# Kernel optimization log

Hardware: AMD Instinct MI355X
Metric: run time of the kernel (lower is better)

The kernel has to match this reference:

```python
import jax, jax.numpy as jnp
import numpy as np

PI = float(np.pi)
C = jnp.complex64
N = 10  # qubits

def m2(a, b, c, d):
    a, b, c, d = jnp.broadcast_arrays(*(jnp.asarray(v, C) for v in (a, b, c, d)))
    return jnp.stack([jnp.stack([a, b], -1), jnp.stack([c, d], -1)], -2)

def rx_mat(t):
    c = jnp.cos(t / 2); s = jnp.sin(t / 2)
    return m2(c, -1j * s, -1j * s, c)

def ry_mat(t):
    c = jnp.cos(t / 2); s = jnp.sin(t / 2)
    return m2(c, -s, s, c)

def rz_mat(t):
    return m2(jnp.exp(-0.5j * t), 0.0, 0.0, jnp.exp(0.5j * t))

def ps_mat(t):
    return m2(1.0, 0.0, 0.0, jnp.exp(1j * t))

def rot_mat(phi, theta, omega):
    c = jnp.cos(theta / 2); s = jnp.sin(theta / 2)
    return m2(jnp.exp(-0.5j * (phi + omega)) * c,
              -jnp.exp(0.5j * (phi - omega)) * s,
              jnp.exp(-0.5j * (phi - omega)) * s,
              jnp.exp(0.5j * (phi + omega)) * c)

def u2_mat(phi, lam):
    r = 1.0 / np.sqrt(2.0)
    return m2(r, -r * jnp.exp(1j * lam), r * jnp.exp(1j * phi), r * jnp.exp(1j * (phi + lam)))

def u3_mat(theta, phi, lam):
    c = jnp.cos(theta / 2); s = jnp.sin(theta / 2)
    return m2(c, -jnp.exp(1j * lam) * s, jnp.exp(1j * phi) * s, jnp.exp(1j * (phi + lam)) * c)

def controlled(U):
    sh = U.shape[:-2]
    I2 = jnp.broadcast_to(jnp.eye(2, dtype=C), sh + (2, 2))
    Z2 = jnp.zeros(sh + (2, 2), C)
    return jnp.concatenate([jnp.concatenate([I2, Z2], -1), jnp.concatenate([Z2, U], -1)], -2)

Y_M = jnp.array([[0, -1j], [1j, 0]], C)
S_M = jnp.array([[1, 0], [0, 1j]], C)
T_M = jnp.array([[1, 0], [0, np.exp(1j * np.pi / 4)]], C)
SX_M = 0.5 * jnp.array([[1 + 1j, 1 - 1j], [1 - 1j, 1 + 1j]], C)
CNOT_M = jnp.array(np.eye(4)[[0, 1, 3, 2]], C)
CZ_M = jnp.array(np.diag([1.0, 1.0, 1.0, -1.0]), C)
CY_M = jnp.array([[1, 0, 0, 0], [0, 1, 0, 0], [0, 0, 0, -1j], [0, 0, 1j, 0]], C)
SWAP_M = jnp.array(np.eye(4)[[0, 2, 1, 3]], C)
CSWAP_M = jnp.array(np.eye(8)[[0, 1, 2, 3, 4, 6, 5, 7]], C)
TOFF_M = jnp.array(np.eye(8)[[0, 1, 2, 3, 4, 5, 7, 6]], C)
CX12_M = jnp.array(np.eye(4)[[0, 1, 3, 2]], C)  # qubitunitary [[1,0,0,0],[0,1,0,0],[0,0,0,1],[0,0,1,0]]

def apply_gate(state, U, wires):
    # state: [B] + [2]*N ; U: [2^k,2^k] or [B,2^k,2^k]
    B = state.shape[0]
    k = len(wires)
    axes = tuple(w + 1 for w in wires)
    s = jnp.moveaxis(state, axes, tuple(range(1, 1 + k)))
    sh = s.shape
    s = s.reshape(B, 2 ** k, -1)
    U = jnp.asarray(U, s.dtype)
    if U.ndim == 2:
        s = jnp.einsum('ij,bjr->bir', U, s)
    else:
        s = jnp.einsum('bij,bjr->bir', U, s)
    return jnp.moveaxis(s.reshape(sh), tuple(range(1, 1 + k)), axes)

def multirz(state, theta, wires):
    # diagonal exp(-i theta/2 * Z...Z) phase
    z = jnp.array([1.0, -1.0], jnp.float32)
    sign = jnp.ones((1,) * (N + 1), jnp.float32)
    for w in wires:
        shp = [1] * (N + 1); shp[w + 1] = 2
        sign = sign * z.reshape(shp)
    theta = jnp.reshape(jnp.asarray(theta), (-1,) + (1,) * N)
    return state * jnp.exp(-0.5j * theta * sign)

def net(x, w1, b1, w2, b2, fw1, fb1, fw2, fb2):
    dn = ('NCHW', 'OIHW', 'NCHW')
    h = jax.lax.conv_general_dilated(x, w1, (1, 1), 'VALID', dimension_numbers=dn)
    h = jax.nn.relu(h + b1[None, :, None, None])
    h = jax.lax.conv_general_dilated(h, w2, (1, 1), 'VALID', dimension_numbers=dn)
    h = jax.nn.relu(h + b2[None, :, None, None])
    h = jax.lax.reduce_window(h, -jnp.inf, jax.lax.max, (1, 1, 2, 2), (1, 1, 2, 2), 'VALID')
    h = h.reshape(h.shape[0], -1)  # [B, 9216]
    h = jax.nn.relu(h @ fw1.T + fb1)
    h = h @ fw2.T + fb2
    return jax.nn.sigmoid(h) * (2.0 * PI)  # angles in [0, 2pi], dropout in eval mode

def run_circuit(ang, q_rx, q_rz3, q_ps6, q_rot7, q_mrz8, q_crx9, q_cry10, q_crz11, q_u2, q_u3):
    B = ang.shape[0]
    state = jnp.zeros((B, 2 ** N), C).at[:, 0].set(1.0).reshape((B,) + (2,) * N)
    for k in range(N):  # TrainableOpAll(RX)
        state = apply_gate(state, rx_mat(q_rx[k]), (k,))
    for k in range(N):  # OpAll(RY) + repeated rx(wire0, x[:,0])
        state = apply_gate(state, ry_mat(ang[:, k]), (k,))
        state = apply_gate(state, rx_mat(ang[:, 0]), (0,))
    for k in range(N - 1):  # TQAll CNOT ring
        state = apply_gate(state, CNOT_M, (k, k + 1))
    state = apply_gate(state, CNOT_M, (N - 1, 0))
    state = apply_gate(state, rx_mat(ang[:, 1]), (1,))
    state = apply_gate(state, rx_mat(jnp.float32(-PI / 4)), (5,))  # q_layer2 fixed
    state = apply_gate(state, ry_mat(ang[:, 2]), (2,))
    state = apply_gate(state, rz_mat(ang[:, 3]), (3,))
    state = apply_gate(state, S_M, (4,))
    state = apply_gate(state, T_M, (5,))
    state = apply_gate(state, rz_mat(q_rz3[0]), (6,))
    state = apply_gate(state, SX_M, (7,))
    # q_device1 (3-wire) ops do not affect the output -> omitted
    state = apply_gate(state, CZ_M, (0, 5))
    state = apply_gate(state, CNOT_M, (0, 5))
    state = apply_gate(state, CY_M, (0, 5))
    state = apply_gate(state, CY_M, (3, 8))
    state = apply_gate(state, SWAP_M, (2, 3))
    state = apply_gate(state, CSWAP_M, (4, 5, 6))
    state = apply_gate(state, TOFF_M, (8, 5, 0))
    state = apply_gate(state, ps_mat(q_ps6[0]), (8,))
    state = apply_gate(state, ps_mat(ang[:, 7]), (7,))
    state = apply_gate(state, rot_mat(q_rot7[0], q_rot7[1], q_rot7[2]), (4,))
    state = apply_gate(state, rot_mat(ang[:, 6], ang[:, 7], ang[:, 8]), (5,))
    state = multirz(state, q_mrz8[0], (2, 3, 4, 5, 6))
    state = multirz(state, ang[:, 5], (3, 4, 6, 7, 8))
    state = apply_gate(state, controlled(rx_mat(ang[:, 6])), (0, 1))
    state = apply_gate(state, controlled(rx_mat(q_crx9[0])), (4, 5))
    state = apply_gate(state, controlled(ry_mat(ang[:, 6])), (0, 1))
    state = apply_gate(state, controlled(ry_mat(q_cry10[0])), (4, 5))
    state = apply_gate(state, controlled(rz_mat(ang[:, 6])), (0, 1))
    state = apply_gate(state, controlled(rz_mat(q_crz11[0])), (4, 5))
    state = apply_gate(state, controlled(rot_mat(jnp.float32(-PI / 4), jnp.float32(PI / 4), jnp.float32(PI / 2))), (5, 6))
    state = apply_gate(state, controlled(rot_mat(ang[:, 5], ang[:, 6], ang[:, 7])), (7, 8))
    state = apply_gate(state, ps_mat(jnp.float32(PI / 7)), (1,))  # U1 == PhaseShift
    state = apply_gate(state, ps_mat(ang[:, 9]), (2,))
    state = apply_gate(state, u2_mat(q_u2[0], q_u2[1]), (8,))
    state = apply_gate(state, u2_mat(ang[:, 0], ang[:, 1]), (4,))
    state = apply_gate(state, u3_mat(q_u3[0], q_u3[1], q_u3[2]), (5,))
    state = apply_gate(state, u3_mat(ang[:, 4], ang[:, 5], ang[:, 6]), (5,))
    # q_layer16 QubitUnitary is identity -> no-op
    state = apply_gate(state, CX12_M, (1, 2))
    red = tuple(range(1, N + 1))
    evs = [jnp.real(jnp.sum(jnp.conj(state) * apply_gate(state, Y_M, (w,)), axis=red)) for w in range(N)]
    return jnp.stack(evs, 1)  # [B, 10]

def setup_inputs():
    key = jax.random.key(0)
    ks = jax.random.split(key, 16)
    B = 1024
    return {
        'x': jax.random.uniform(ks[0], (B, 1, 28, 28), jnp.float32),
        'conv1_w': jax.random.normal(ks[1], (32, 1, 3, 3), jnp.float32) * 0.2,
        'conv1_b': jnp.zeros((32,), jnp.float32),
        'conv2_w': jax.random.normal(ks[2], (64, 32, 3, 3), jnp.float32) * 0.05,
        'conv2_b': jnp.zeros((64,), jnp.float32),
        'fc1_w': jax.random.normal(ks[3], (128, 9216), jnp.float32) * 0.01,
        'fc1_b': jnp.zeros((128,), jnp.float32),
        'fc2_w': jax.random.normal(ks[4], (10, 128), jnp.float32) * 0.08,
        'fc2_b': jnp.zeros((10,), jnp.float32),
        'q_rx': jax.random.uniform(ks[5], (10,), jnp.float32, 0.0, 2 * PI),
        'q_rz3': jax.random.uniform(ks[6], (1,), jnp.float32, 0.0, 2 * PI),
        'q_ps6': jax.random.uniform(ks[7], (1,), jnp.float32, 0.0, 2 * PI),
        'q_rot7': jax.random.uniform(ks[8], (3,), jnp.float32, 0.0, 2 * PI),
        'q_mrz8': jax.random.uniform(ks[9], (1,), jnp.float32, 0.0, 2 * PI),
        'q_crx9': jax.random.uniform(ks[10], (1,), jnp.float32, 0.0, 2 * PI),
        'q_cry10': jax.random.uniform(ks[11], (1,), jnp.float32, 0.0, 2 * PI),
        'q_crz11': jax.random.uniform(ks[12], (1,), jnp.float32, 0.0, 2 * PI),
        'q_u2_14': jnp.array([PI / 7, PI / 8.8], jnp.float32),
        'q_u3_15': jax.random.uniform(ks[13], (3,), jnp.float32, 0.0, 2 * PI),
    }

def reference(x, conv1_w, conv1_b, conv2_w, conv2_b, fc1_w, fc1_b, fc2_w, fc2_b,
              q_rx, q_rz3, q_ps6, q_rot7, q_mrz8, q_crx9, q_cry10, q_crz11, q_u2_14, q_u3_15):
    ang = net(x, conv1_w, conv1_b, conv2_w, conv2_b, fc1_w, fc1_b, fc2_w, fc2_b)
    ev = run_circuit(ang, q_rx, q_rz3, q_ps6, q_rot7, q_mrz8, q_crx9, q_cry10, q_crz11, q_u2_14, q_u3_15)
    return jax.nn.log_softmax(ev, axis=1)
```

## Files before the change

### kernel.cpp

```cpp
#include <hip/hip_runtime.h>
#include <hip/hip_bf16.h>

#define PI_F 3.14159265358979323846f

__global__ void Static_82300163326800_kernel() {}

typedef _Float16 f16x8 __attribute__((ext_vector_type(8)));
typedef _Float16 f16x4 __attribute__((ext_vector_type(4)));
typedef float f32x4 __attribute__((ext_vector_type(4)));

struct M2 { float2 m00, m01, m10, m11; };

__device__ __forceinline__ int ins1(int x, int p) {
    return ((x >> p) << (p + 1)) | (x & ((1 << p) - 1));
}
__device__ __forceinline__ M2 mrx(float th) {
    float s, c; __sincosf(0.5f * th, &s, &c);
    return { make_float2(c,0.f), make_float2(0.f,-s), make_float2(0.f,-s), make_float2(c,0.f) };
}
__device__ __forceinline__ M2 mry(float th) {
    float s, c; __sincosf(0.5f * th, &s, &c);
    return { make_float2(c,0.f), make_float2(-s,0.f), make_float2(s,0.f), make_float2(c,0.f) };
}
__device__ __forceinline__ M2 mrot(float phi, float th, float om) {
    float s, c;  __sincosf(0.5f * th, &s, &c);
    float sa, ca; __sincosf(0.5f * (phi + om), &sa, &ca);
    float sd, cd; __sincosf(0.5f * (phi - om), &sd, &cd);
    return { make_float2(ca*c, -sa*c), make_float2(-cd*s, -sd*s),
             make_float2(cd*s, -sd*s), make_float2(ca*c,  sa*c) };
}
__device__ __forceinline__ M2 mu2(float phi, float lam) {
    const float r = 0.7071067811865476f;
    float sl, cl;   __sincosf(lam, &sl, &cl);
    float sp, cp;   __sincosf(phi, &sp, &cp);
    float spl, cpl; __sincosf(phi + lam, &spl, &cpl);
    return { make_float2(r,0.f), make_float2(-r*cl,-r*sl),
             make_float2(r*cp, r*sp), make_float2(r*cpl, r*spl) };
}
__device__ __forceinline__ M2 mu3(float th, float phi, float lam) {
    float s, c;     __sincosf(0.5f * th, &s, &c);
    float sl, cl;   __sincosf(lam, &sl, &cl);
    float sp, cp;   __sincosf(phi, &sp, &cp);
    float spl, cpl; __sincosf(phi + lam, &spl, &cpl);
    return { make_float2(c,0.f), make_float2(-cl*s,-sl*s),
             make_float2(cp*s, sp*s), make_float2(cpl*c, spl*c) };
}
__device__ __forceinline__ void apply1(float2* st, int t, int w, M2 m) {
    int p = 9 - w;
    int i0 = ins1(t, p), i1 = i0 | (1 << p);
    float2 a = st[i0], d = st[i1];
    st[i0] = make_float2(m.m00.x*a.x - m.m00.y*a.y + m.m01.x*d.x - m.m01.y*d.y,
                         m.m00.x*a.y + m.m00.y*a.x + m.m01.x*d.y + m.m01.y*d.x);
    st[i1] = make_float2(m.m10.x*a.x - m.m10.y*a.y + m.m11.x*d.x - m.m11.y*d.y,
                         m.m10.x*a.y + m.m10.y*a.x + m.m11.x*d.y + m.m11.y*d.x);
}
__device__ __forceinline__ void diag1(float2* st, int t, int w, float2 d0, float2 d1) {
    int p = 9 - w;
    int i0 = ins1(t, p), i1 = i0 | (1 << p);
    float2 a = st[i0], c = st[i1];
    st[i0] = make_float2(d0.x*a.x - d0.y*a.y, d0.x*a.y + d0.y*a.x);
    st[i1] = make_float2(d1.x*c.x - d1.y*c.y, d1.x*c.y + d1.y*c.x);
}
__device__ __forceinline__ void capply1(float2* st, int t, int c, int w, M2 m) {
    if (t < 256) {
        int pc = 9 - c, pw = 9 - w;
        int pl = pc < pw ? pc : pw, ph = pc + pw - pl;
        int base = ins1(ins1(t, pl), ph) | (1 << pc);
        int i0 = base, i1 = base | (1 << pw);
        float2 a = st[i0], d = st[i1];
        st[i0] = make_float2(m.m00.x*a.x - m.m00.y*a.y + m.m01.x*d.x - m.m01.y*d.y,
                             m.m00.x*a.y + m.m00.y*a.x + m.m01.x*d.y + m.m01.y*d.x);
        st[i1] = make_float2(m.m10.x*a.x - m.m10.y*a.y + m.m11.x*d.x - m.m11.y*d.y,
                             m.m10.x*a.y + m.m10.y*a.x + m.m11.x*d.y + m.m11.y*d.x);
    }
}
__device__ __forceinline__ void cdiag1(float2* st, int t, int c, int w, float2 d0, float2 d1) {
    if (t < 256) {
        int pc = 9 - c, pw = 9 - w;
        int pl = pc < pw ? pc : pw, ph = pc + pw - pl;
        int base = ins1(ins1(t, pl), ph) | (1 << pc);
        int i0 = base, i1 = base | (1 << pw);
        float2 a = st[i0], e = st[i1];
        st[i0] = make_float2(d0.x*a.x - d0.y*a.y, d0.x*a.y + d0.y*a.x);
        st[i1] = make_float2(d1.x*e.x - d1.y*e.y, d1.x*e.y + d1.y*e.x);
    }
}
__device__ __forceinline__ void cnotg(float2* st, int t, int c, int w) {
    if (t < 256) {
        int pc = 9 - c, pw = 9 - w;
        int pl = pc < pw ? pc : pw, ph = pc + pw - pl;
        int base = ins1(ins1(t, pl), ph) | (1 << pc);
        int i1 = base | (1 << pw);
        float2 a = st[base]; st[base] = st[i1]; st[i1] = a;
    }
}
__device__ __forceinline__ void czg(float2* st, int t, int c, int w) {
    if (t < 256) {
        int pc = 9 - c, pw = 9 - w;
        int pl = pc < pw ? pc : pw, ph = pc + pw - pl;
        int i = ins1(ins1(t, pl), ph) | (1 << pc) | (1 << pw);
        st[i] = make_float2(-st[i].x, -st[i].y);
    }
}
__device__ __forceinline__ void swapg(float2* st, int t, int a, int b_) {
    if (t < 256) {
        int pa = 9 - a, pb = 9 - b_;
        int pl = pa < pb ? pa : pb, ph = pa + pb - pl;
        int base = ins1(ins1(t, pl), ph);
        int iA = base | (1 << pa), iB = base | (1 << pb);
        float2 u = st[iA]; st[iA] = st[iB]; st[iB] = u;
    }
}
__device__ __forceinline__ void cswap456(float2* st, int t) {
    if (t < 128) {
        int base = ins1(ins1(ins1(t, 3), 4), 5) | (1 << 5);
        int iA = base | (1 << 4), iB = base | (1 << 3);
        float2 u = st[iA]; st[iA] = st[iB]; st[iB] = u;
    }
}
__device__ __forceinline__ void toff850(float2* st, int t) {
    if (t < 128) {
        int base = ins1(ins1(ins1(t, 1), 4), 9) | (1 << 1) | (1 << 4);
        int i1 = base | (1 << 9);
        float2 u = st[base]; st[base] = st[i1]; st[i1] = u;
    }
}
__device__ __forceinline__ void mrzg(float2* st, int t, int mask, float th) {
    float sh, ch; __sincosf(0.5f * th, &sh, &ch);
#pragma unroll
    for (int q = 0; q < 2; ++q) {
        int i = t + q * 512;
        float sg = (__popc(i & mask) & 1) ? sh : -sh;
        float2 a = st[i];
        st[i] = make_float2(ch*a.x - sg*a.y, ch*a.y + sg*a.x);
    }
}

__device__ __forceinline__ void run_circ(
    float2* st, float (*red)[10], float* evs, int t, const float* ang,
    const float* q_rx, const float* q_rz3, const float* q_ps6, const float* q_rot7,
    const float* q_mrz8, const float* q_crx9, const float* q_cry10, const float* q_crz11,
    const float* q_u2, const float* q_u3, float* outf)
{
    st[t] = make_float2(t == 0 ? 1.f : 0.f, 0.f);
    st[t + 512] = make_float2(0.f, 0.f);

#pragma unroll
    for (int k = 0; k < 10; ++k) { M2 m = mrx(q_rx[k]); __syncthreads(); apply1(st, t, k, m); }
    {
        M2 mx0 = mrx(ang[0]);
#pragma unroll
        for (int k = 0; k < 10; ++k) {
            M2 m = mry(ang[k]); __syncthreads(); apply1(st, t, k, m);
            __syncthreads(); apply1(st, t, 0, mx0);
        }
    }
#pragma unroll
    for (int k = 0; k < 9; ++k) { __syncthreads(); cnotg(st, t, k, k + 1); }
    __syncthreads(); cnotg(st, t, 9, 0);

    { M2 m = mrx(ang[1]);      __syncthreads(); apply1(st, t, 1, m); }
    { M2 m = mrx(-PI_F / 4.f); __syncthreads(); apply1(st, t, 5, m); }
    { M2 m = mry(ang[2]);      __syncthreads(); apply1(st, t, 2, m); }
    { float s, c; __sincosf(0.5f * ang[3], &s, &c);
      __syncthreads(); diag1(st, t, 3, make_float2(c,-s), make_float2(c,s)); }
    __syncthreads(); diag1(st, t, 4, make_float2(1.f,0.f), make_float2(0.f,1.f));
    __syncthreads(); diag1(st, t, 5, make_float2(1.f,0.f),
                           make_float2(0.7071067811865476f, 0.7071067811865476f));
    { float s, c; __sincosf(0.5f * q_rz3[0], &s, &c);
      __syncthreads(); diag1(st, t, 6, make_float2(c,-s), make_float2(c,s)); }
    { M2 m = { make_float2(0.5f,0.5f), make_float2(0.5f,-0.5f),
               make_float2(0.5f,-0.5f), make_float2(0.5f,0.5f) };
      __syncthreads(); apply1(st, t, 7, m); }
    __syncthreads(); czg(st, t, 0, 5);
    __syncthreads(); cnotg(st, t, 0, 5);
    { M2 y = { make_float2(0.f,0.f), make_float2(0.f,-1.f),
               make_float2(0.f,1.f), make_float2(0.f,0.f) };
      __syncthreads(); capply1(st, t, 0, 5, y);
      __syncthreads(); capply1(st, t, 3, 8, y); }
    __syncthreads(); swapg(st, t, 2, 3);
    __syncthreads(); cswap456(st, t);
    __syncthreads(); toff850(st, t);
    { float s, c; __sincosf(q_ps6[0], &s, &c);
      __syncthreads(); diag1(st, t, 8, make_float2(1.f,0.f), make_float2(c,s)); }
    { float s, c; __sincosf(ang[7], &s, &c);
      __syncthreads(); diag1(st, t, 7, make_float2(1.f,0.f), make_float2(c,s)); }
    { M2 m = mrot(q_rot7[0], q_rot7[1], q_rot7[2]); __syncthreads(); apply1(st, t, 4, m); }
    { M2 m = mrot(ang[6], ang[7], ang[8]);          __syncthreads(); apply1(st, t, 5, m); }
    __syncthreads(); mrzg(st, t, 0xF8, q_mrz8[0]);
    __syncthreads(); mrzg(st, t, 0x6E, ang[5]);
    { M2 m = mrx(ang[6]);      __syncthreads(); capply1(st, t, 0, 1, m); }
    { M2 m = mrx(q_crx9[0]);   __syncthreads(); capply1(st, t, 4, 5, m); }
    { M2 m = mry(ang[6]);      __syncthreads(); capply1(st, t, 0, 1, m); }
    { M2 m = mry(q_cry10[0]);  __syncthreads(); capply1(st, t, 4, 5, m); }
    { float s, c; __sincosf(0.5f * ang[6], &s, &c);
      __syncthreads(); cdiag1(st, t, 0, 1, make_float2(c,-s), make_float2(c,s)); }
    { float s, c; __sincosf(0.5f * q_crz11[0], &s, &c);
      __syncthreads(); cdiag1(st, t, 4, 5, make_float2(c,-s), make_float2(c,s)); }
    { M2 m = mrot(-PI_F/4.f, PI_F/4.f, PI_F/2.f); __syncthreads(); capply1(st, t, 5, 6, m); }
    { M2 m = mrot(ang[5], ang[6], ang[7]);        __syncthreads(); capply1(st, t, 7, 8, m); }
    { float s, c; __sincosf(PI_F/7.f, &s, &c);
      __syncthreads(); diag1(st, t, 1, make_float2(1.f,0.f), make_float2(c,s)); }
    { float s, c; __sincosf(ang[9], &s, &c);
      __syncthreads(); diag1(st, t, 2, make_float2(1.f,0.f), make_float2(c,s)); }
    { M2 m = mu2(q_u2[0], q_u2[1]); __syncthreads(); apply1(st, t, 8, m); }
    { M2 m = mu2(ang[0], ang[1]);   __syncthreads(); apply1(st, t, 4, m); }
    { M2 m = mu3(q_u3[0], q_u3[1], q_u3[2]); __syncthreads(); apply1(st, t, 5, m); }
    { M2 m = mu3(ang[4], ang[5], ang[6]);    __syncthreads(); apply1(st, t, 5, m); }
    __syncthreads(); cnotg(st, t, 1, 2);
    __syncthreads();

    float loc[10];
#pragma unroll
    for (int w = 0; w < 10; ++w) {
        int p = 9 - w;
        int i0 = ins1(t, p), i1 = i0 | (1 << p);
        float2 a = st[i0], c = st[i1];
        loc[w] = 2.f * (a.x * c.y - a.y * c.x);
    }
    int lane = t & 63, wv = t >> 6;
#pragma unroll
    for (int w = 0; w < 10; ++w) {
        float v = loc[w];
        v += __shfl_down(v, 32); v += __shfl_down(v, 16); v += __shfl_down(v, 8);
        v += __shfl_down(v, 4);  v += __shfl_down(v, 2);  v += __shfl_down(v, 1);
        if (lane == 0) red[wv][w] = v;
    }
    __syncthreads();
    if (t < 10) {
        float e = 0.f;
#pragma unroll
        for (int i = 0; i < 8; ++i) e += red[i][t];
        evs[t] = e;
    }
    __syncthreads();
    if (t < 10) {
        float mx = evs[0];
#pragma unroll
        for (int i = 1; i < 10; ++i) mx = fmaxf(mx, evs[i]);
        float ss = 0.f;
#pragma unroll
        for (int i = 0; i < 10; ++i) ss += expf(evs[i] - mx);
        outf[t] = evs[t] - mx - logf(ss);
    }
}

__global__ __launch_bounds__(256) void prep_w2(
    const float* __restrict__ w2, _Float16* __restrict__ w2t)
{
    int idx = blockIdx.x * 256 + threadIdx.x;
    if (idx < 18432) {
        int oc = idx / 288, r = idx - oc * 288;
        int s = r >> 5, ic = r & 31;
        w2t[idx] = (_Float16)w2[oc * 288 + ic * 9 + s];
    }
}

__global__ __launch_bounds__(256) void prep_fw1(
    const float* __restrict__ fw1, _Float16* __restrict__ out)
{
    int i = blockIdx.x * 256 + threadIdx.x;
    if (i < 294912) {
        float4 v = ((const float4*)fw1)[i];
        f16x4 o = { (_Float16)v.x, (_Float16)v.y, (_Float16)v.z, (_Float16)v.w };
        *(f16x4*)(out + i * 4) = o;
    }
}

__global__ __launch_bounds__(256, 2) void convnet_mfma(
    const float* __restrict__ x, const float* __restrict__ w1, const float* __restrict__ b1,
    const _Float16* __restrict__ w2t, const float* __restrict__ b2,
    _Float16* __restrict__ flat)
{
    __shared__ float xs[784];
    __shared__ float w1s[288];
    __shared__ __align__(16) _Float16 h1t[676 * 40];
    const int n = blockIdx.x, t = threadIdx.x;
    const int lane = t & 63, wv = t >> 6;
    const int m = lane & 15, quad = lane >> 4;

    for (int i = t; i < 784; i += 256) xs[i] = x[n * 784 + i];
    for (int i = t; i < 288; i += 256) w1s[i] = w1[i];

    bf16x8_dummy: ;
    f16x8 bq[9][4];
#pragma unroll
    for (int s = 0; s < 9; ++s)
#pragma unroll
        for (int nt = 0; nt < 4; ++nt)
            bq[s][nt] = *(const f16x8*)(w2t + (nt * 16 + m) * 288 + s * 32 + quad * 8);

    __syncthreads();

    {
        const int ic = t & 31;
        float wr[9];
#pragma unroll
        for (int k = 0; k < 9; ++k) wr[k] = w1s[ic * 9 + k];
        const float bb = b1[ic];
        for (int pix = (t >> 5); pix < 676; pix += 8) {
            int yy = pix / 26, xx = pix - yy * 26;
            const float* xp = xs + yy * 28 + xx;
            float s = bb;
            s += xp[0]*wr[0]  + xp[1]*wr[1]  + xp[2]*wr[2]
               + xp[28]*wr[3] + xp[29]*wr[4] + xp[30]*wr[5]
               + xp[56]*wr[6] + xp[57]*wr[7] + xp[58]*wr[8];
            h1t[pix * 40 + ic] = (_Float16)fmaxf(s, 0.f);
        }
    }
    __syncthreads();

    float bb2[4];
#pragma unroll
    for (int nt = 0; nt < 4; ++nt) bb2[nt] = b2[nt * 16 + m];

    _Float16* outp = flat + (size_t)n * 9216;

    for (int q = 0; q < 9; ++q) {
        const int mt = wv + q * 4;
        const int a = mt / 3, b3 = mt - a * 3;
        const int y0 = 2 * a + (m & 1), x0 = 8 * b3 + (m >> 1);
        f32x4 acc[4] = {};
#pragma unroll
        for (int s = 0; s < 9; ++s) {
            const int ky = s / 3, kx = s - ky * 3;
            f16x8 af = *(const f16x8*)&h1t[((y0 + ky) * 26 + x0 + kx) * 40 + quad * 8];
#pragma unroll
            for (int nt = 0; nt < 4; ++nt)
                acc[nt] = __builtin_amdgcn_mfma_f32_16x16x32_f16(af, bq[s][nt], acc[nt], 0, 0, 0);
        }
        const int pooled_idx = a * 12 + 4 * b3 + quad;
#pragma unroll
        for (int nt = 0; nt < 4; ++nt) {
            float v = fmaxf(fmaxf(acc[nt][0], acc[nt][1]), fmaxf(acc[nt][2], acc[nt][3]));
            outp[(nt * 16 + m) * 144 + pooled_idx] = (_Float16)fmaxf(v + bb2[nt], 0.f);
        }
    }
}

__global__ __launch_bounds__(256) void fc1_mfma(
    const _Float16* __restrict__ A, const _Float16* __restrict__ B, float* __restrict__ part)
{
    const int m0 = blockIdx.x * 64, n0 = blockIdx.y * 64, kb = blockIdx.z;
    const int t = threadIdx.x, lane = t & 63, wv = t >> 6;
    const int r = lane & 15, quad = lane >> 4;
    const _Float16* ap = A + (size_t)(m0 + wv * 16 + r) * 9216 + kb * 576 + quad * 8;
    const _Float16* bp = B + (size_t)(n0 + r) * 9216 + kb * 576 + quad * 8;
    f32x4 acc[4] = {};
    for (int ks = 0; ks < 576; ks += 32) {
        f16x8 af = *(const f16x8*)(ap + ks);
#pragma unroll
        for (int nt = 0; nt < 4; ++nt) {
            f16x8 bfr = *(const f16x8*)(bp + (size_t)nt * 16 * 9216 + ks);
            acc[nt] = __builtin_amdgcn_mfma_f32_16x16x32_f16(af, bfr, acc[nt], 0, 0, 0);
        }
    }
    float* pp = part + (size_t)kb * 131072 + (size_t)(m0 + wv * 16 + quad * 4) * 128 + n0 + r;
#pragma unroll
    for (int nt = 0; nt < 4; ++nt)
#pragma unroll
        for (int reg = 0; reg < 4; ++reg)
            pp[reg * 128 + nt * 16] = acc[nt][reg];
}

__global__ __launch_bounds__(128) void fc2_kernel(
    const float* __restrict__ part, const float* __restrict__ fb1,
    const float* __restrict__ fw2, const float* __restrict__ fb2, float* __restrict__ angO)
{
    __shared__ float h[128];
    const int b = blockIdx.x, t = threadIdx.x;
    float s = fb1[t];
#pragma unroll
    for (int kb = 0; kb < 16; ++kb) s += part[(size_t)kb * 131072 + b * 128 + t];
    h[t] = fmaxf(s, 0.f);
    __syncthreads();
    if (t < 10) {
        float d = fb2[t];
#pragma unroll 16
        for (int k = 0; k < 128; ++k) d += h[k] * fw2[t * 128 + k];
        angO[b * 10 + t] = 6.283185307179586f / (1.f + expf(-d));
    }
}

__global__ __launch_bounds__(512) void circuit_kernel(
    const float* __restrict__ ang_g,
    const float* __restrict__ q_rx, const float* __restrict__ q_rz3,
    const float* __restrict__ q_ps6, const float* __restrict__ q_rot7,
    const float* __restrict__ q_mrz8, const float* __restrict__ q_crx9,
    const float* __restrict__ q_cry10, const float* __restrict__ q_crz11,
    const float* __restrict__ q_u2, const float* __restrict__ q_u3,
    float* __restrict__ out)
{
    __shared__ float2 st[1024];
    __shared__ float red[8][10];
    __shared__ float evs[10];
    const int b = blockIdx.x, t = threadIdx.x;
    float a[10];
#pragma unroll
    for (int j = 0; j < 10; ++j) a[j] = ang_g[b * 10 + j];
    run_circ(st, red, evs, t, a, q_rx, q_rz3, q_ps6, q_rot7, q_mrz8,
             q_crx9, q_cry10, q_crz11, q_u2, q_u3, out + b * 10);
}

template <int NT>
__device__ __forceinline__ void conv_stage(
    float* buf, int n, int t,
    const float* __restrict__ x, const float* __restrict__ w1, const float* __restrict__ b1,
    const float* __restrict__ w2, const float* __restrict__ b2)
{
    float* xs  = buf;
    float* w1s = buf + 784;
    float* h1s = buf + 1072;
    float* w2s = buf + 1748;
    const int ocq = t / 24, r = t - ocq * 24;
    const bool active = (t < 384);

    for (int i = t; i < 784; i += NT) xs[i] = x[n * 784 + i];
    for (int i = t; i < 288; i += NT) w1s[i] = w1[i];

    float acc[4][24];
#pragma unroll
    for (int j = 0; j < 4; ++j)
#pragma unroll
        for (int xo = 0; xo < 24; ++xo) acc[j][xo] = 0.f;

    for (int ic = 0; ic < 32; ++ic) {
        __syncthreads();
        float bb1 = b1[ic];
        for (int i = t; i < 676; i += NT) {
            int yy = i / 26, xx = i - yy * 26;
            const float* xp = xs + yy * 28 + xx;
            const float* wp = w1s + ic * 9;
            float s = bb1;
#pragma unroll
            for (int ky = 0; ky < 3; ++ky)
#pragma unroll
                for (int kx = 0; kx < 3; ++kx)
                    s += xp[ky * 28 + kx] * wp[ky * 3 + kx];
            h1s[i] = fmaxf(s, 0.f);
        }
        for (int i = t; i < 576; i += NT) {
            int oc = i / 9, k = i - oc * 9;
            w2s[i] = w2[oc * 288 + ic * 9 + k];
        }
        __syncthreads();
        if (active) {
            float wr[4][9];
#pragma unroll
            for (int j = 0; j < 4; ++j)
#pragma unroll
                for (int k = 0; k < 9; ++k)
                    wr[j][k] = w2s[(ocq * 4 + j) * 9 + k];
            float c0[3], c1[3];
#pragma unroll
            for (int q = 0; q < 3; ++q) { c0[q] = h1s[(r + q) * 26]; c1[q] = h1s[(r + q) * 26 + 1]; }
#pragma unroll
            for (int xo = 0; xo < 24; ++xo) {
                float c2[3];
#pragma unroll
                for (int q = 0; q < 3; ++q) c2[q] = h1s[(r + q) * 26 + xo + 2];
#pragma unroll
                for (int j = 0; j < 4; ++j) {
                    acc[j][xo] += wr[j][0]*c0[0] + wr[j][1]*c1[0] + wr[j][2]*c2[0]
                                + wr[j][3]*c0[1] + wr[j][4]*c1[1] + wr[j][5]*c2[1]
                                + wr[j][6]*c0[2] + wr[j][7]*c1[2] + wr[j][8]*c2[2];
                }
#pragma unroll
                for (int q = 0; q < 3; ++q) { c0[q] = c1[q]; c1[q] = c2[q]; }
            }
        }
    }
    __syncthreads();
    if (active && (r & 1)) {
#pragma unroll
        for (int j = 0; j < 4; ++j) {
            int oc = ocq * 4 + j;
            float bb = b2[oc];
#pragma unroll
            for (int px = 0; px < 12; ++px) {
                float v0 = fmaxf(acc[j][2*px]   + bb, 0.f);
                float v1 = fmaxf(acc[j][2*px+1] + bb, 0.f);
                buf[oc * 144 + (r >> 1) * 12 + px] = fmaxf(v0, v1);
            }
        }
    }
    __syncthreads();
    if (active && !(r & 1)) {
#pragma unroll
        for (int j = 0; j < 4; ++j) {
            int oc = ocq * 4 + j;
            float bb = b2[oc];
#pragma unroll
            for (int px = 0; px < 12; ++px) {
                float v0 = fmaxf(acc[j][2*px]   + bb, 0.f);
                float v1 = fmaxf(acc[j][2*px+1] + bb, 0.f);
                int idx = oc * 144 + (r >> 1) * 12 + px;
                buf[idx] = fmaxf(fmaxf(v0, v1), buf[idx]);
            }
        }
    }
    __syncthreads();
}

__global__ __launch_bounds__(512) void fused_kernel(
    const float* __restrict__ x, const float* __restrict__ w1, const float* __restrict__ b1,
    const float* __restrict__ w2, const float* __restrict__ b2,
    const float* __restrict__ fw1, const float* __restrict__ fb1,
    const float* __restrict__ fw2, const float* __restrict__ fb2,
    const float* __restrict__ q_rx, const float* __restrict__ q_rz3,
    const float* __restrict__ q_ps6, const float* __restrict__ q_rot7,
    const float* __restrict__ q_mrz8, const float* __restrict__ q_crx9,
    const float* __restrict__ q_cry10, const float* __restrict__ q_crz11,
    const float* __restrict__ q_u2, const float* __restrict__ q_u3,
    float* __restrict__ out)
{
    __shared__ float buf[9216];
    __shared__ float2 st[1024];
    __shared__ float hred[512];
    __shared__ float hvec[128];
    __shared__ float angs[10];
    __shared__ float red[8][10];
    __shared__ float evs[10];
    const int n = blockIdx.x, t = threadIdx.x;

    conv_stage<512>(buf, n, t, x, w1, b1, w2, b2);

    {
        const int j = t >> 2, q = t & 3;
        const float* wrow = fw1 + (size_t)j * 9216 + q * 2304;
        const float* arow = buf + q * 2304;
        float s = 0.f;
        for (int k = 0; k < 2304; k += 4) {
            float4 w = *(const float4*)(wrow + k);
            s += w.x * arow[k] + w.y * arow[k+1] + w.z * arow[k+2] + w.w * arow[k+3];
        }
        hred[t] = s;
    }
    __syncthreads();
    if (t < 128)
        hvec[t] = fmaxf(fb1[t] + hred[t*4] + hred[t*4+1] + hred[t*4+2] + hred[t*4+3], 0.f);
    __syncthreads();
    if (t < 10) {
        float d = fb2[t];
#pragma unroll 16
        for (int k = 0; k < 128; ++k) d += hvec[k] * fw2[t * 128 + k];
        angs[t] = 6.283185307179586f / (1.f + expf(-d));
    }
    __syncthreads();
    run_circ(st, red, evs, t, angs, q_rx, q_rz3, q_ps6, q_rot7, q_mrz8,
             q_crx9, q_cry10, q_crz11, q_u2, q_u3, out + n * 10);
}

extern "C" void kernel_launch(void* const* d_in, const int* in_sizes, int n_in,
                              void* d_out, int out_size, void* d_ws, size_t ws_size,
                              hipStream_t stream)
{
    (void)in_sizes; (void)n_in;
    const float* x    = (const float*)d_in[0];
    const float* w1   = (const float*)d_in[1];
    const float* b1   = (const float*)d_in[2];
    const float* w2   = (const float*)d_in[3];
    const float* b2   = (const float*)d_in[4];
    const float* fw1  = (const float*)d_in[5];
    const float* fb1  = (const float*)d_in[6];
    const float* fw2  = (const float*)d_in[7];
    const float* fb2  = (const float*)d_in[8];
    const float* qrx  = (const float*)d_in[9];
    const float* qrz3 = (const float*)d_in[10];
    const float* qps6 = (const float*)d_in[11];
    const float* qrot7 = (const float*)d_in[12];
    const float* qmrz8 = (const float*)d_in[13];
    const float* qcrx9 = (const float*)d_in[14];
    const float* qcry10 = (const float*)d_in[15];
    const float* qcrz11 = (const float*)d_in[16];
    const float* qu2  = (const float*)d_in[17];
    const float* qu3  = (const float*)d_in[18];
    float* out = (float*)d_out;

    const size_t flat_bytes = (size_t)1024 * 9216 * 2;
    const size_t part_bytes = (size_t)16 * 1024 * 128 * 4;
    const size_t ang_bytes  = (size_t)1024 * 10 * 4;
    const size_t w2t_bytes  = (size_t)18432 * 2;
    const size_t fw1h_bytes = (size_t)128 * 9216 * 2;
    const size_t o_flat = 0;
    const size_t o_part = o_flat + flat_bytes;
    const size_t o_ang  = o_part + part_bytes;
    const size_t o_w2t  = o_ang + ang_bytes;
    const size_t o_fw1h = o_w2t + w2t_bytes;
    const size_t need   = o_fw1h + fw1h_bytes;

    (void)hipGetLastError();

    if (ws_size >= need) {
        _Float16* flat = (_Float16*)((char*)d_ws + o_flat);
        float*    part = (float*)((char*)d_ws + o_part);
        float*    angb = (float*)((char*)d_ws + o_ang);
        _Float16* w2t  = (_Float16*)((char*)d_ws + o_w2t);
        _Float16* fw1h = (_Float16*)((char*)d_ws + o_fw1h);
        prep_w2<<<72, 256, 0, stream>>>(w2, w2t);
        prep_fw1<<<1152, 256, 0, stream>>>(fw1, fw1h);
        convnet_mfma<<<1024, 256, 0, stream>>>(x, w1, b1, w2t, b2, flat);
        fc1_mfma<<<dim3(16, 2, 16), 256, 0, stream>>>(flat, fw1h, part);
        fc2_kernel<<<1024, 128, 0, stream>>>(part, fb1, fw2, fb2, angb);
        circuit_kernel<<<1024, 512, 0, stream>>>(angb, qrx, qrz3, qps6, qrot7, qmrz8,
                                                 qcrx9, qcry10, qcrz11, qu2, qu3, out);
    } else {
        fused_kernel<<<1024, 512, 0, stream>>>(x, w1, b1, w2, b2, fw1, fb1, fw2, fb2,
                                               qrx, qrz3, qps6, qrot7, qmrz8,
                                               qcrx9, qcry10, qcrz11, qu2, qu3, out);
    }
    if (hipGetLastError() != hipSuccess) {
        (void)hipMemsetAsync(d_out, 0x7F, (size_t)out_size * 2, stream);
    }
}
```

Before: 204.8 us.

## Simulate quantum circuit per wavefront in registers with lane shuffles

Replaces the 512-thread shared-memory circuit kernel, which had a __syncthreads between every gate, with one 64-lane wavefront per sample. Each lane holds 16 amplitudes in registers: the high six qubits map to lane bits and the low four to register indices. Gates become xor-shuffles or in-register permutations, so block-wide barriers and LDS traffic go away. The conv1 stage is also changed to a sliding-window row computation. The cost is hand-derived mappings for every gate, which raises the risk of correctness errors.

```diff
diff --git a/kernel.cpp b/kernel.cpp
--- a/kernel.cpp
+++ b/kernel.cpp
@@ -11,8 +11,14 @@
 
 struct M2 { float2 m00, m01, m10, m11; };
 
-__device__ __forceinline__ int ins1(int x, int p) {
-    return ((x >> p) << (p + 1)) | (x & ((1 << p) - 1));
+__device__ __forceinline__ float2 cmul2(float2 a, float2 b) {
+    return make_float2(a.x*b.x - a.y*b.y, a.x*b.y + a.y*b.x);
+}
+__device__ __forceinline__ float2 cadd2(float2 a, float2 b) {
+    return make_float2(a.x+b.x, a.y+b.y);
+}
+__device__ __forceinline__ float2 shx(float2 v, int m) {
+    return make_float2(__shfl_xor(v.x, m), __shfl_xor(v.y, m));
 }
 __device__ __forceinline__ M2 mrx(float th) {
     float s, c; __sincosf(0.5f * th, &s, &c);
@@ -45,21 +51,505 @@
     return { make_float2(c,0.f), make_float2(-cl*s,-sl*s),
              make_float2(cp*s, sp*s), make_float2(cpl*c, spl*c) };
 }
+
+
+__device__ __forceinline__ void applyL(float2* s, M2 m, int lane, int q) {
+    const int bitv = (lane >> q) & 1;
+    const float2 cA = bitv ? m.m11 : m.m00;
+    const float2 cB = bitv ? m.m10 : m.m01;
+#pragma unroll
+    for (int r = 0; r < 16; ++r) {
+        float2 o = shx(s[r], 1 << q);
+        s[r] = cadd2(cmul2(cA, s[r]), cmul2(cB, o));
+    }
+}
+template<int P>
+__device__ __forceinline__ void applyR(float2* s, M2 m) {
+#pragma unroll
+    for (int r0 = 0; r0 < 16; ++r0) {
+        if (r0 & (1 << P)) continue;
+        const int r1 = r0 | (1 << P);
+        float2 a = s[r0], d = s[r1];
+        s[r0] = cadd2(cmul2(m.m00, a), cmul2(m.m01, d));
+        s[r1] = cadd2(cmul2(m.m10, a), cmul2(m.m11, d));
+    }
+}
+__device__ __forceinline__ void diagL(float2* s, float2 d0, float2 d1, int lane, int q) {
+    const int bitv = (lane >> q) & 1;
+    const float2 f = bitv ? d1 : d0;
+#pragma unroll
+    for (int r = 0; r < 16; ++r) s[r] = cmul2(f, s[r]);
+}
+template<int P>
+__device__ __forceinline__ void diagR(float2* s, float2 d0, float2 d1) {
+#pragma unroll
+    for (int r = 0; r < 16; ++r) {
+        const float2 f = (r & (1 << P)) ? d1 : d0;
+        s[r] = cmul2(f, s[r]);
+    }
+}
+__device__ __forceinline__ void cnotLL(float2* s, int lane, int qc, int qw) {
+    const int cb = (lane >> qc) & 1;
+#pragma unroll
+    for (int r = 0; r < 16; ++r) {
+        float2 o = shx(s[r], 1 << qw);
+        s[r] = cb ? o : s[r];
+    }
+}
+__device__ __forceinline__ void capplyLL(float2* s, M2 m, int lane, int qc, int qw) {
+    const int cb = (lane >> qc) & 1, tb = (lane >> qw) & 1;
+    float2 cA = tb ? m.m11 : m.m00;
+    float2 cB = tb ? m.m10 : m.m01;
+    cA = cb ? cA : make_float2(1.f, 0.f);
+    cB = cb ? cB : make_float2(0.f, 0.f);
+#pragma unroll
+    for (int r = 0; r < 16; ++r) {
+        float2 o = shx(s[r], 1 << qw);
+        s[r] = cadd2(cmul2(cA, s[r]), cmul2(cB, o));
+    }
+}
+__device__ __forceinline__ void cdiagLL(float2* s, float2 d0, float2 d1, int lane, int qc, int qw) {
+    const int cb = (lane >> qc) & 1, tb = (lane >> qw) & 1;
+    float2 f = tb ? d1 : d0;
+    f = cb ? f : make_float2(1.f, 0.f);
+#pragma unroll
+    for (int r = 0; r < 16; ++r) s[r] = cmul2(f, s[r]);
+}
+template<int P>
+__device__ __forceinline__ void capplyRL(float2* s, M2 m, int lane, int qc) {
+    const int cb = (lane >> qc) & 1;
+#pragma unroll
+    for (int r0 = 0; r0 < 16; ++r0) {
+        if (r0 & (1 << P)) continue;
+        const int r1 = r0 | (1 << P);
+        float2 a = s[r0], d = s[r1];
+        float2 na = cadd2(cmul2(m.m00, a), cmul2(m.m01, d));
+        float2 nd = cadd2(cmul2(m.m10, a), cmul2(m.m11, d));
+        s[r0] = cb ? na : a;
+        s[r1] = cb ? nd : d;
+    }
+}
+
+__global__ __launch_bounds__(256) void circuit_wave(
+    const float* __restrict__ ang_g,
+    const float* __restrict__ q_rx, const float* __restrict__ q_rz3,
+    const float* __restrict__ q_ps6, const float* __restrict__ q_rot7,
+    const float* __restrict__ q_mrz8, const float* __restrict__ q_crx9,
+    const float* __restrict__ q_cry10, const float* __restrict__ q_crz11,
+    const float* __restrict__ q_u2, const float* __restrict__ q_u3,
+    float* __restrict__ out)
+{
+    const int t = threadIdx.x, lane = t & 63, wv = t >> 6;
+    const int b = blockIdx.x * 4 + wv;
+    float ang[10];
+#pragma unroll
+    for (int j = 0; j < 10; ++j) ang[j] = ang_g[b * 10 + j];
+
+    float2 s[16];
+#pragma unroll
+    for (int r = 0; r < 16; ++r) s[r] = make_float2(0.f, 0.f);
+    if (lane == 0) s[0].x = 1.f;
+
+    applyL(s, mrx(q_rx[0]), lane, 5);
+    applyL(s, mrx(q_rx[1]), lane, 4);
+    applyL(s, mrx(q_rx[2]), lane, 3);
+    applyL(s, mrx(q_rx[3]), lane, 2);
+    applyL(s, mrx(q_rx[4]), lane, 1);
+    applyL(s, mrx(q_rx[5]), lane, 0);
+    applyR<3>(s, mrx(q_rx[6]));
+    applyR<2>(s, mrx(q_rx[7]));
+    applyR<1>(s, mrx(q_rx[8]));
+    applyR<0>(s, mrx(q_rx[9]));
+    {
+        M2 mx0 = mrx(ang[0]);
+        applyL(s, mry(ang[0]), lane, 5); applyL(s, mx0, lane, 5);
+        applyL(s, mry(ang[1]), lane, 4); applyL(s, mx0, lane, 5);
+        applyL(s, mry(ang[2]), lane, 3); applyL(s, mx0, lane, 5);
+        applyL(s, mry(ang[3]), lane, 2); applyL(s, mx0, lane, 5);
+        applyL(s, mry(ang[4]), lane, 1); applyL(s, mx0, lane, 5);
+        applyL(s, mry(ang[5]), lane, 0); applyL(s, mx0, lane, 5);
+        applyR<3>(s, mry(ang[6]));       applyL(s, mx0, lane, 5);
+        applyR<2>(s, mry(ang[7]));       applyL(s, mx0, lane, 5);
+        applyR<1>(s, mry(ang[8]));       applyL(s, mx0, lane, 5);
+        applyR<0>(s, mry(ang[9]));       applyL(s, mx0, lane, 5);
+    }
+    cnotLL(s, lane, 5, 4);
+    cnotLL(s, lane, 4, 3);
+    cnotLL(s, lane, 3, 2);
+    cnotLL(s, lane, 2, 1);
+    cnotLL(s, lane, 1, 0);
+    {
+        const int cb = lane & 1;
+#pragma unroll
+        for (int r0 = 0; r0 < 8; ++r0) {
+            float2 a = s[r0], d = s[r0 + 8];
+            s[r0] = cb ? d : a; s[r0 + 8] = cb ? a : d;
+        }
+    }
+    {
+        float2 u;
+        u = s[8];  s[8]  = s[12]; s[12] = u;
+        u = s[9];  s[9]  = s[13]; s[13] = u;
+        u = s[10]; s[10] = s[14]; s[14] = u;
+        u = s[11]; s[11] = s[15]; s[15] = u;
+    }
+    {
+        float2 u;
+        u = s[4];  s[4]  = s[6];  s[6]  = u;
+        u = s[5];  s[5]  = s[7];  s[7]  = u;
+        u = s[12]; s[12] = s[14]; s[14] = u;
+        u = s[13]; s[13] = s[15]; s[15] = u;
+    }
+    {
+        float2 u;
+        u = s[2];  s[2]  = s[3];  s[3]  = u;
+        u = s[6];  s[6]  = s[7];  s[7]  = u;
+        u = s[10]; s[10] = s[11]; s[11] = u;
+        u = s[14]; s[14] = s[15]; s[15] = u;
+    }
+    {
+#pragma unroll
+        for (int r = 1; r < 16; r += 2) { float2 o = shx(s[r], 32); s[r] = o; }
+    }
+
+    applyL(s, mrx(ang[1]), lane, 4);
+    applyL(s, mrx(-PI_F / 4.f), lane, 0);
+    applyL(s, mry(ang[2]), lane, 3);
+    { float sn, cs; __sincosf(0.5f * ang[3], &sn, &cs);
+      diagL(s, make_float2(cs,-sn), make_float2(cs,sn), lane, 2); }
+    diagL(s, make_float2(1.f,0.f), make_float2(0.f,1.f), lane, 1);
+    diagL(s, make_float2(1.f,0.f),
+          make_float2(0.7071067811865476f, 0.7071067811865476f), lane, 0);
+    { float sn, cs; __sincosf(0.5f * q_rz3[0], &sn, &cs);
+      diagR<3>(s, make_float2(cs,-sn), make_float2(cs,sn)); }
+    { M2 m = { make_float2(0.5f,0.5f), make_float2(0.5f,-0.5f),
+               make_float2(0.5f,-0.5f), make_float2(0.5f,0.5f) };
+      applyR<2>(s, m); }
+    {
+        const float sgn = (((lane >> 5) & 1) && (lane & 1)) ? -1.f : 1.f;
+#pragma unroll
+        for (int r = 0; r < 16; ++r) { s[r].x *= sgn; s[r].y *= sgn; }
+    }
+    cnotLL(s, lane, 5, 0);
+    {
+        const int cb = (lane >> 5) & 1, tb = lane & 1;
+#pragma unroll
+        for (int r = 0; r < 16; ++r) {
+            float2 o = shx(s[r], 1);
+            float2 val = tb ? make_float2(-o.y, o.x) : make_float2(o.y, -o.x);
+            s[r] = cb ? val : s[r];
+        }
+    }
+    {
+        const int cb = (lane >> 2) & 1;
+#pragma unroll
+        for (int r0 = 0; r0 < 16; ++r0) {
+            if (r0 & 2) continue;
+            const int r1 = r0 | 2;
+            float2 a = s[r0], d = s[r1];
+            float2 na = make_float2(d.y, -d.x);
+            float2 nd = make_float2(-a.y, a.x);
+            s[r0] = cb ? na : a; s[r1] = cb ? nd : d;
+        }
+    }
+    {
+        const int pr = ((lane >> 3) & 1) ^ ((lane >> 2) & 1);
+#pragma unroll
+        for (int r = 0; r < 16; ++r) {
+            float2 o = shx(s[r], 12);
+            s[r] = pr ? o : s[r];
+        }
+    }
+    {
+        float2 o16[16];
+#pragma unroll
+        for (int r = 0; r < 16; ++r) o16[r] = shx(s[r ^ 8], 1);
+        const int cb = (lane >> 1) & 1, lb = lane & 1;
+#pragma unroll
+        for (int r = 0; r < 16; ++r) {
+            const int pr = cb & ((r & 8) ? (1 - lb) : lb);
+            s[r] = pr ? o16[r] : s[r];
+        }
+    }
+    {
+        const int lb = lane & 1;
+#pragma unroll
+        for (int r = 0; r < 16; ++r) {
+            if (!(r & 2)) continue;
+            float2 o = shx(s[r], 32);
+            s[r] = lb ? o : s[r];
+        }
+    }
+    { float sn, cs; __sincosf(q_ps6[0], &sn, &cs);
+      diagR<1>(s, make_float2(1.f,0.f), make_float2(cs,sn)); }
+    { float sn, cs; __sincosf(ang[7], &sn, &cs);
+      diagR<2>(s, make_float2(1.f,0.f), make_float2(cs,sn)); }
+    applyL(s, mrot(q_rot7[0], q_rot7[1], q_rot7[2]), lane, 1);
+    applyL(s, mrot(ang[6], ang[7], ang[8]), lane, 0);
+    {
+        float sh, ch; __sincosf(0.5f * q_mrz8[0], &sh, &ch);
+        const int lp = __popc(lane & 0xF) & 1;
+        const float sg0 = lp ? sh : -sh;
+#pragma unroll
+        for (int r = 0; r < 16; ++r) {
+            const float sg = (r & 8) ? -sg0 : sg0;
+            float2 a = s[r];
+            s[r] = make_float2(ch*a.x - sg*a.y, ch*a.y + sg*a.x);
+        }
+    }
+    {
+        float sh, ch; __sincosf(0.5f * ang[5], &sh, &ch);
+        const int lp = __popc(lane & 6) & 1;
+        const float sg0 = lp ? sh : -sh;
+#pragma unroll
+        for (int r = 0; r < 16; ++r) {
+            const int rp = __popc(r & 14) & 1;
+            const float sg = rp ? -sg0 : sg0;
+            float2 a = s[r];
+            s[r] = make_float2(ch*a.x - sg*a.y, ch*a.y + sg*a.x);
+        }
+    }
+    capplyLL(s, mrx(ang[6]), lane, 5, 4);
+    capplyLL(s, mrx(q_crx9[0]), lane, 1, 0);
+    capplyLL(s, mry(ang[6]), lane, 5, 4);
+    capplyLL(s, mry(q_cry10[0]), lane, 1, 0);
+    { float sn, cs; __sincosf(0.5f * ang[6], &sn, &cs);
+      cdiagLL(s, make_float2(cs,-sn), make_float2(cs,sn), lane, 5, 4); }
+    { float sn, cs; __sincosf(0.5f * q_crz11[0], &sn, &cs);
+      cdiagLL(s, make_float2(cs,-sn), make_float2(cs,sn), lane, 1, 0); }
+    capplyRL<3>(s, mrot(-PI_F/4.f, PI_F/4.f, PI_F/2.f), lane, 0);
+    {
+        M2 m = mrot(ang[5], ang[6], ang[7]);
+        const int idx4[4] = {4, 5, 12, 13};
+#pragma unroll
+        for (int k = 0; k < 4; ++k) {
+            const int r0 = idx4[k], r1 = r0 | 2;
+            float2 a = s[r0], d = s[r1];
+            s[r0] = cadd2(cmul2(m.m00, a), cmul2(m.m01, d));
+            s[r1] = cadd2(cmul2(m.m10, a), cmul2(m.m11, d));
+        }
+    }
+    { float sn, cs; __sincosf(PI_F / 7.f, &sn, &cs);
+      diagL(s, make_float2(1.f,0.f), make_float2(cs,sn), lane, 4); }
+    { float sn, cs; __sincosf(ang[9], &sn, &cs);
+      diagL(s, make_float2(1.f,0.f), make_float2(cs,sn), lane, 3); }
+    applyR<1>(s, mu2(q_u2[0], q_u2[1]));
+    applyL(s, mu2(ang[0], ang[1]), lane, 1);
+    applyL(s, mu3(q_u3[0], q_u3[1], q_u3[2]), lane, 0);
+    applyL(s, mu3(ang[4], ang[5], ang[6]), lane, 0);
+    cnotLL(s, lane, 4, 3);
+
+    float ev[10];
+#pragma unroll
+    for (int w = 0; w < 6; ++w) {
+        const int q = 5 - w;
+        const int bitv = (lane >> q) & 1;
+        float acc = 0.f;
+#pragma unroll
+        for (int r = 0; r < 16; ++r) {
+            float2 o = shx(s[r], 1 << q);
+            acc += s[r].x * o.y - s[r].y * o.x;
+        }
+        ev[w] = bitv ? 0.f : 2.f * acc;
+    }
+#pragma unroll
+    for (int w = 6; w < 10; ++w) {
+        const int P = 9 - w;
+        float acc = 0.f;
+#pragma unroll
+        for (int r0 = 0; r0 < 16; ++r0) {
+            if (r0 & (1 << P)) continue;
+            const int r1 = r0 | (1 << P);
+            acc += s[r0].x * s[r1].y - s[r0].y * s[r1].x;
+        }
+        ev[w] = 2.f * acc;
+    }
+#pragma unroll
+    for (int w = 0; w < 10; ++w) {
+        float v = ev[w];
+        v += __shfl_down(v, 32); v += __shfl_down(v, 16); v += __shfl_down(v, 8);
+        v += __shfl_down(v, 4);  v += __shfl_down(v, 2);  v += __shfl_down(v, 1);
+        ev[w] = v;
+    }
+    if (lane == 0) {
+        float mx = ev[0];
+#pragma unroll
+        for (int i = 1; i < 10; ++i) mx = fmaxf(mx, ev[i]);
+        float ss = 0.f;
+#pragma unroll
+        for (int i = 0; i < 10; ++i) ss += expf(ev[i] - mx);
+        const float ls = logf(ss);
+#pragma unroll
+        for (int i = 0; i < 10; ++i) out[b * 10 + i] = ev[i] - mx - ls;
+    }
+}
+
+__global__ __launch_bounds__(256) void prep_w2(
+    const float* __restrict__ w2, _Float16* __restrict__ w2t)
+{
+    int idx = blockIdx.x * 256 + threadIdx.x;
+    if (idx < 18432) {
+        int oc = idx / 288, r = idx - oc * 288;
+        int s = r >> 5, ic = r & 31;
+        w2t[idx] = (_Float16)w2[oc * 288 + ic * 9 + s];
+    }
+}
+
+__global__ __launch_bounds__(256) void prep_fw1(
+    const float* __restrict__ fw1, _Float16* __restrict__ out)
+{
+    int i = blockIdx.x * 256 + threadIdx.x;
+    if (i < 294912) {
+        float4 v = ((const float4*)fw1)[i];
+        f16x4 o = { (_Float16)v.x, (_Float16)v.y, (_Float16)v.z, (_Float16)v.w };
+        *(f16x4*)(out + i * 4) = o;
+    }
+}
+
+__global__ __launch_bounds__(256, 2) void convnet_mfma(
+    const float* __restrict__ x, const float* __restrict__ w1, const float* __restrict__ b1,
+    const _Float16* __restrict__ w2t, const float* __restrict__ b2,
+    _Float16* __restrict__ flat)
+{
+    __shared__ float xs[784];
+    __shared__ float w1s[288];
+    __shared__ __align__(16) _Float16 h1t[676 * 40];
+    const int n = blockIdx.x, t = threadIdx.x;
+    const int lane = t & 63, wv = t >> 6;
+    const int m = lane & 15, quad = lane >> 4;
+
+    for (int i = t; i < 784; i += 256) xs[i] = x[n * 784 + i];
+    for (int i = t; i < 288; i += 256) w1s[i] = w1[i];
+
+    f16x8 bq[9][4];
+#pragma unroll
+    for (int s = 0; s < 9; ++s)
+#pragma unroll
+        for (int nt = 0; nt < 4; ++nt)
+            bq[s][nt] = *(const f16x8*)(w2t + (nt * 16 + m) * 288 + s * 32 + quad * 8);
+
+    __syncthreads();
+
+    {
+        const int ic = t & 31, j = t >> 5;
+        float wr[9];
+#pragma unroll
+        for (int k = 0; k < 9; ++k) wr[k] = w1s[ic * 9 + k];
+        const float bb = b1[ic];
+        for (int pg = j; pg < 13; pg += 8) {
+            const int y0 = 2 * pg;
+            float p0[4], p1[4];
+#pragma unroll
+            for (int k = 0; k < 4; ++k) {
+                p0[k] = xs[(y0 + k) * 28];
+                p1[k] = xs[(y0 + k) * 28 + 1];
+            }
+            for (int xx = 0; xx < 26; ++xx) {
+                float n2[4];
+#pragma unroll
+                for (int k = 0; k < 4; ++k) n2[k] = xs[(y0 + k) * 28 + xx + 2];
+                float s0 = bb, s1 = bb;
+#pragma unroll
+                for (int ky = 0; ky < 3; ++ky) {
+                    s0 += p0[ky] * wr[3*ky] + p1[ky] * wr[3*ky+1] + n2[ky] * wr[3*ky+2];
+                    s1 += p0[ky+1] * wr[3*ky] + p1[ky+1] * wr[3*ky+1] + n2[ky+1] * wr[3*ky+2];
+                }
+                h1t[(y0 * 26 + xx) * 40 + ic]       = (_Float16)fmaxf(s0, 0.f);
+                h1t[((y0 + 1) * 26 + xx) * 40 + ic] = (_Float16)fmaxf(s1, 0.f);
+#pragma unroll
+                for (int k = 0; k < 4; ++k) { p0[k] = p1[k]; p1[k] = n2[k]; }
+            }
+        }
+    }
+    __syncthreads();
+
+    float bb2[4];
+#pragma unroll
+    for (int nt = 0; nt < 4; ++nt) bb2[nt] = b2[nt * 16 + m];
+
+    _Float16* outp = flat + (size_t)n * 9216;
+
+    for (int q = 0; q < 9; ++q) {
+        const int mt = wv + q * 4;
+        const int a = mt / 3, b3 = mt - a * 3;
+        const int y0 = 2 * a + (m & 1), x0 = 8 * b3 + (m >> 1);
+        f32x4 acc[4] = {};
+#pragma unroll
+        for (int s = 0; s < 9; ++s) {
+            const int ky = s / 3, kx = s - ky * 3;
+            f16x8 af = *(const f16x8*)&h1t[((y0 + ky) * 26 + x0 + kx) * 40 + quad * 8];
+#pragma unroll
+            for (int nt = 0; nt < 4; ++nt)
+                acc[nt] = __builtin_amdgcn_mfma_f32_16x16x32_f16(af, bq[s][nt], acc[nt], 0, 0, 0);
+        }
+        const int pooled_idx = a * 12 + 4 * b3 + quad;
+#pragma unroll
+        for (int nt = 0; nt < 4; ++nt) {
+            float v = fmaxf(fmaxf(acc[nt][0], acc[nt][1]), fmaxf(acc[nt][2], acc[nt][3]));
+            outp[(nt * 16 + m) * 144 + pooled_idx] = (_Float16)fmaxf(v + bb2[nt], 0.f);
+        }
+    }
+}
+
+__global__ __launch_bounds__(256) void fc1_mfma(
+    const _Float16* __restrict__ A, const _Float16* __restrict__ B, float* __restrict__ part)
+{
+    const int m0 = blockIdx.x * 64, n0 = blockIdx.y * 64, kb = blockIdx.z;
+    const int t = threadIdx.x, lane = t & 63, wv = t >> 6;
+    const int r = lane & 15, quad = lane >> 4;
+    const _Float16* ap = A + (size_t)(m0 + wv * 16 + r) * 9216 + kb * 576 + quad * 8;
+    const _Float16* bp = B + (size_t)(n0 + r) * 9216 + kb * 576 + quad * 8;
+    f32x4 acc[4] = {};
+    for (int ks = 0; ks < 576; ks += 32) {
+        f16x8 af = *(const f16x8*)(ap + ks);
+#pragma unroll
+        for (int nt = 0; nt < 4; ++nt) {
+            f16x8 bfr = *(const f16x8*)(bp + (size_t)nt * 16 * 9216 + ks);
+            acc[nt] = __builtin_amdgcn_mfma_f32_16x16x32_f16(af, bfr, acc[nt], 0, 0, 0);
+        }
+    }
+    float* pp = part + (size_t)kb * 131072 + (size_t)(m0 + wv * 16 + quad * 4) * 128 + n0 + r;
+#pragma unroll
+    for (int nt = 0; nt < 4; ++nt)
+#pragma unroll
+        for (int reg = 0; reg < 4; ++reg)
+            pp[reg * 128 + nt * 16] = acc[nt][reg];
+}
+
+__global__ __launch_bounds__(128) void fc2_kernel(
+    const float* __restrict__ part, const float* __restrict__ fb1,
+    const float* __restrict__ fw2, const float* __restrict__ fb2, float* __restrict__ angO)
+{
+    __shared__ float h[128];
+    const int b = blockIdx.x, t = threadIdx.x;
+    float s = fb1[t];
+#pragma unroll
+    for (int kb = 0; kb < 16; ++kb) s += part[(size_t)kb * 131072 + b * 128 + t];
+    h[t] = fmaxf(s, 0.f);
+    __syncthreads();
+    if (t < 10) {
+        float d = fb2[t];
+#pragma unroll 16
+        for (int k = 0; k < 128; ++k) d += h[k] * fw2[t * 128 + k];
+        angO[b * 10 + t] = 6.283185307179586f / (1.f + expf(-d));
+    }
+}
+
+__device__ __forceinline__ int ins1(int x, int p) {
+    return ((x >> p) << (p + 1)) | (x & ((1 << p) - 1));
+}
 __device__ __forceinline__ void apply1(float2* st, int t, int w, M2 m) {
     int p = 9 - w;
     int i0 = ins1(t, p), i1 = i0 | (1 << p);
     float2 a = st[i0], d = st[i1];
-    st[i0] = make_float2(m.m00.x*a.x - m.m00.y*a.y + m.m01.x*d.x - m.m01.y*d.y,
-                         m.m00.x*a.y + m.m00.y*a.x + m.m01.x*d.y + m.m01.y*d.x);
-    st[i1] = make_float2(m.m10.x*a.x - m.m10.y*a.y + m.m11.x*d.x - m.m11.y*d.y,
-                         m.m10.x*a.y + m.m10.y*a.x + m.m11.x*d.y + m.m11.y*d.x);
+    st[i0] = cadd2(cmul2(m.m00, a), cmul2(m.m01, d));
+    st[i1] = cadd2(cmul2(m.m10, a), cmul2(m.m11, d));
 }
 __device__ __forceinline__ void diag1(float2* st, int t, int w, float2 d0, float2 d1) {
     int p = 9 - w;
     int i0 = ins1(t, p), i1 = i0 | (1 << p);
-    float2 a = st[i0], c = st[i1];
-    st[i0] = make_float2(d0.x*a.x - d0.y*a.y, d0.x*a.y + d0.y*a.x);
-    st[i1] = make_float2(d1.x*c.x - d1.y*c.y, d1.x*c.y + d1.y*c.x);
+    st[i0] = cmul2(d0, st[i0]);
+    st[i1] = cmul2(d1, st[i1]);
 }
 __device__ __forceinline__ void capply1(float2* st, int t, int c, int w, M2 m) {
     if (t < 256) {
@@ -68,10 +558,8 @@
         int base = ins1(ins1(t, pl), ph) | (1 << pc);
         int i0 = base, i1 = base | (1 << pw);
         float2 a = st[i0], d = st[i1];
-        st[i0] = make_float2(m.m00.x*a.x - m.m00.y*a.y + m.m01.x*d.x - m.m01.y*d.y,
-                             m.m00.x*a.y + m.m00.y*a.x + m.m01.x*d.y + m.m01.y*d.x);
-        st[i1] = make_float2(m.m10.x*a.x - m.m10.y*a.y + m.m11.x*d.x - m.m11.y*d.y,
-                             m.m10.x*a.y + m.m10.y*a.x + m.m11.x*d.y + m.m11.y*d.x);
+        st[i0] = cadd2(cmul2(m.m00, a), cmul2(m.m01, d));
+        st[i1] = cadd2(cmul2(m.m10, a), cmul2(m.m11, d));
     }
 }
 __device__ __forceinline__ void cdiag1(float2* st, int t, int c, int w, float2 d0, float2 d1) {
@@ -79,10 +567,8 @@
         int pc = 9 - c, pw = 9 - w;
         int pl = pc < pw ? pc : pw, ph = pc + pw - pl;
         int base = ins1(ins1(t, pl), ph) | (1 << pc);
-        int i0 = base, i1 = base | (1 << pw);
-        float2 a = st[i0], e = st[i1];
-        st[i0] = make_float2(d0.x*a.x - d0.y*a.y, d0.x*a.y + d0.y*a.x);
-        st[i1] = make_float2(d1.x*e.x - d1.y*e.y, d1.x*e.y + d1.y*e.x);
+        st[base] = cmul2(d0, st[base]);
+        st[base | (1 << pw)] = cmul2(d1, st[base | (1 << pw)]);
     }
 }
 __device__ __forceinline__ void cnotg(float2* st, int t, int c, int w) {
@@ -111,14 +597,14 @@
         float2 u = st[iA]; st[iA] = st[iB]; st[iB] = u;
     }
 }
-__device__ __forceinline__ void cswap456(float2* st, int t) {
+__device__ __forceinline__ void cswap456f(float2* st, int t) {
     if (t < 128) {
         int base = ins1(ins1(ins1(t, 3), 4), 5) | (1 << 5);
         int iA = base | (1 << 4), iB = base | (1 << 3);
         float2 u = st[iA]; st[iA] = st[iB]; st[iB] = u;
     }
 }
-__device__ __forceinline__ void toff850(float2* st, int t) {
+__device__ __forceinline__ void toff850f(float2* st, int t) {
     if (t < 128) {
         int base = ins1(ins1(ins1(t, 1), 4), 9) | (1 << 1) | (1 << 4);
         int i1 = base | (1 << 9);
@@ -135,7 +621,6 @@
         st[i] = make_float2(ch*a.x - sg*a.y, ch*a.y + sg*a.x);
     }
 }
-
 __device__ __forceinline__ void run_circ(
     float2* st, float (*red)[10], float* evs, int t, const float* ang,
     const float* q_rx, const float* q_rz3, const float* q_ps6, const float* q_rot7,
@@ -144,7 +629,6 @@
 {
     st[t] = make_float2(t == 0 ? 1.f : 0.f, 0.f);
     st[t + 512] = make_float2(0.f, 0.f);
-
 #pragma unroll
     for (int k = 0; k < 10; ++k) { M2 m = mrx(q_rx[k]); __syncthreads(); apply1(st, t, k, m); }
     {
@@ -158,7 +642,6 @@
 #pragma unroll
     for (int k = 0; k < 9; ++k) { __syncthreads(); cnotg(st, t, k, k + 1); }
     __syncthreads(); cnotg(st, t, 9, 0);
-
     { M2 m = mrx(ang[1]);      __syncthreads(); apply1(st, t, 1, m); }
     { M2 m = mrx(-PI_F / 4.f); __syncthreads(); apply1(st, t, 5, m); }
     { M2 m = mry(ang[2]);      __syncthreads(); apply1(st, t, 2, m); }
@@ -179,8 +662,8 @@
       __syncthreads(); capply1(st, t, 0, 5, y);
       __syncthreads(); capply1(st, t, 3, 8, y); }
     __syncthreads(); swapg(st, t, 2, 3);
-    __syncthreads(); cswap456(st, t);
-    __syncthreads(); toff850(st, t);
+    __syncthreads(); cswap456f(st, t);
+    __syncthreads(); toff850f(st, t);
     { float s, c; __sincosf(q_ps6[0], &s, &c);
       __syncthreads(); diag1(st, t, 8, make_float2(1.f,0.f), make_float2(c,s)); }
     { float s, c; __sincosf(ang[7], &s, &c);
@@ -209,7 +692,6 @@
     { M2 m = mu3(ang[4], ang[5], ang[6]);    __syncthreads(); apply1(st, t, 5, m); }
     __syncthreads(); cnotg(st, t, 1, 2);
     __syncthreads();
-
     float loc[10];
 #pragma unroll
     for (int w = 0; w < 10; ++w) {
@@ -218,13 +700,13 @@
         float2 a = st[i0], c = st[i1];
         loc[w] = 2.f * (a.x * c.y - a.y * c.x);
     }
-    int lane = t & 63, wv = t >> 6;
+    int lane = t & 63, wvv = t >> 6;
 #pragma unroll
     for (int w = 0; w < 10; ++w) {
         float v = loc[w];
         v += __shfl_down(v, 32); v += __shfl_down(v, 16); v += __shfl_down(v, 8);
         v += __shfl_down(v, 4);  v += __shfl_down(v, 2);  v += __shfl_down(v, 1);
-        if (lane == 0) red[wv][w] = v;
+        if (lane == 0) red[wvv][w] = v;
     }
     __syncthreads();
     if (t < 10) {
@@ -244,164 +726,6 @@
         outf[t] = evs[t] - mx - logf(ss);
     }
 }
-
-__global__ __launch_bounds__(256) void prep_w2(
-    const float* __restrict__ w2, _Float16* __restrict__ w2t)
-{
-    int idx = blockIdx.x * 256 + threadIdx.x;
-    if (idx < 18432) {
-        int oc = idx / 288, r = idx - oc * 288;
-        int s = r >> 5, ic = r & 31;
-        w2t[idx] = (_Float16)w2[oc * 288 + ic * 9 + s];
-    }
-}
-
-__global__ __launch_bounds__(256) void prep_fw1(
-    const float* __restrict__ fw1, _Float16* __restrict__ out)
-{
-    int i = blockIdx.x * 256 + threadIdx.x;
-    if (i < 294912) {
-        float4 v = ((const float4*)fw1)[i];
-        f16x4 o = { (_Float16)v.x, (_Float16)v.y, (_Float16)v.z, (_Float16)v.w };
-        *(f16x4*)(out + i * 4) = o;
-    }
-}
-
-__global__ __launch_bounds__(256, 2) void convnet_mfma(
-    const float* __restrict__ x, const float* __restrict__ w1, const float* __restrict__ b1,
-    const _Float16* __restrict__ w2t, const float* __restrict__ b2,
-    _Float16* __restrict__ flat)
-{
-    __shared__ float xs[784];
-    __shared__ float w1s[288];
-    __shared__ __align__(16) _Float16 h1t[676 * 40];
-    const int n = blockIdx.x, t = threadIdx.x;
-    const int lane = t & 63, wv = t >> 6;
-    const int m = lane & 15, quad = lane >> 4;
-
-    for (int i = t; i < 784; i += 256) xs[i] = x[n * 784 + i];
-    for (int i = t; i < 288; i += 256) w1s[i] = w1[i];
-
-    bf16x8_dummy: ;
-    f16x8 bq[9][4];
-#pragma unroll
-    for (int s = 0; s < 9; ++s)
-#pragma unroll
-        for (int nt = 0; nt < 4; ++nt)
-            bq[s][nt] = *(const f16x8*)(w2t + (nt * 16 + m) * 288 + s * 32 + quad * 8);
-
-    __syncthreads();
-
-    {
-        const int ic = t & 31;
-        float wr[9];
-#pragma unroll
-        for (int k = 0; k < 9; ++k) wr[k] = w1s[ic * 9 + k];
-        const float bb = b1[ic];
-        for (int pix = (t >> 5); pix < 676; pix += 8) {
-            int yy = pix / 26, xx = pix - yy * 26;
-            const float* xp = xs + yy * 28 + xx;
-            float s = bb;
-            s += xp[0]*wr[0]  + xp[1]*wr[1]  + xp[2]*wr[2]
-               + xp[28]*wr[3] + xp[29]*wr[4] + xp[30]*wr[5]
-               + xp[56]*wr[6] + xp[57]*wr[7] + xp[58]*wr[8];
-            h1t[pix * 40 + ic] = (_Float16)fmaxf(s, 0.f);
-        }
-    }
-    __syncthreads();
-
-    float bb2[4];
-#pragma unroll
-    for (int nt = 0; nt < 4; ++nt) bb2[nt] = b2[nt * 16 + m];
-
-    _Float16* outp = flat + (size_t)n * 9216;
-
-    for (int q = 0; q < 9; ++q) {
-        const int mt = wv + q * 4;
-        const int a = mt / 3, b3 = mt - a * 3;
-        const int y0 = 2 * a + (m & 1), x0 = 8 * b3 + (m >> 1);
-        f32x4 acc[4] = {};
-#pragma unroll
-        for (int s = 0; s < 9; ++s) {
-            const int ky = s / 3, kx = s - ky * 3;
-            f16x8 af = *(const f16x8*)&h1t[((y0 + ky) * 26 + x0 + kx) * 40 + quad * 8];
-#pragma unroll
-            for (int nt = 0; nt < 4; ++nt)
-                acc[nt] = __builtin_amdgcn_mfma_f32_16x16x32_f16(af, bq[s][nt], acc[nt], 0, 0, 0);
-        }
-        const int pooled_idx = a * 12 + 4 * b3 + quad;
-#pragma unroll
-        for (int nt = 0; nt < 4; ++nt) {
-            float v = fmaxf(fmaxf(acc[nt][0], acc[nt][1]), fmaxf(acc[nt][2], acc[nt][3]));
-            outp[(nt * 16 + m) * 144 + pooled_idx] = (_Float16)fmaxf(v + bb2[nt], 0.f);
-        }
-    }
-}
-
-__global__ __launch_bounds__(256) void fc1_mfma(
-    const _Float16* __restrict__ A, const _Float16* __restrict__ B, float* __restrict__ part)
-{
-    const int m0 = blockIdx.x * 64, n0 = blockIdx.y * 64, kb = blockIdx.z;
-    const int t = threadIdx.x, lane = t & 63, wv = t >> 6;
-    const int r = lane & 15, quad = lane >> 4;
-    const _Float16* ap = A + (size_t)(m0 + wv * 16 + r) * 9216 + kb * 576 + quad * 8;
-    const _Float16* bp = B + (size_t)(n0 + r) * 9216 + kb * 576 + quad * 8;
-    f32x4 acc[4] = {};
-    for (int ks = 0; ks < 576; ks += 32) {
-        f16x8 af = *(const f16x8*)(ap + ks);
-#pragma unroll
-        for (int nt = 0; nt < 4; ++nt) {
-            f16x8 bfr = *(const f16x8*)(bp + (size_t)nt * 16 * 9216 + ks);
-            acc[nt] = __builtin_amdgcn_mfma_f32_16x16x32_f16(af, bfr, acc[nt], 0, 0, 0);
-        }
-    }
-    float* pp = part + (size_t)kb * 131072 + (size_t)(m0 + wv * 16 + quad * 4) * 128 + n0 + r;
-#pragma unroll
-    for (int nt = 0; nt < 4; ++nt)
-#pragma unroll
-        for (int reg = 0; reg < 4; ++reg)
-            pp[reg * 128 + nt * 16] = acc[nt][reg];
-}
-
-__global__ __launch_bounds__(128) void fc2_kernel(
-    const float* __restrict__ part, const float* __restrict__ fb1,
-    const float* __restrict__ fw2, const float* __restrict__ fb2, float* __restrict__ angO)
-{
-    __shared__ float h[128];
-    const int b = blockIdx.x, t = threadIdx.x;
-    float s = fb1[t];
-#pragma unroll
-    for (int kb = 0; kb < 16; ++kb) s += part[(size_t)kb * 131072 + b * 128 + t];
-    h[t] = fmaxf(s, 0.f);
-    __syncthreads();
-    if (t < 10) {
-        float d = fb2[t];
-#pragma unroll 16
-        for (int k = 0; k < 128; ++k) d += h[k] * fw2[t * 128 + k];
-        angO[b * 10 + t] = 6.283185307179586f / (1.f + expf(-d));
-    }
-}
-
-__global__ __launch_bounds__(512) void circuit_kernel(
-    const float* __restrict__ ang_g,
-    const float* __restrict__ q_rx, const float* __restrict__ q_rz3,
-    const float* __restrict__ q_ps6, const float* __restrict__ q_rot7,
-    const float* __restrict__ q_mrz8, const float* __restrict__ q_crx9,
-    const float* __restrict__ q_cry10, const float* __restrict__ q_crz11,
-    const float* __restrict__ q_u2, const float* __restrict__ q_u3,
-    float* __restrict__ out)
-{
-    __shared__ float2 st[1024];
-    __shared__ float red[8][10];
-    __shared__ float evs[10];
-    const int b = blockIdx.x, t = threadIdx.x;
-    float a[10];
-#pragma unroll
-    for (int j = 0; j < 10; ++j) a[j] = ang_g[b * 10 + j];
-    run_circ(st, red, evs, t, a, q_rx, q_rz3, q_ps6, q_rot7, q_mrz8,
-             q_crx9, q_cry10, q_crz11, q_u2, q_u3, out + b * 10);
-}
-
 template <int NT>
 __device__ __forceinline__ void conv_stage(
     float* buf, int n, int t,
@@ -414,16 +738,13 @@
     float* w2s = buf + 1748;
     const int ocq = t / 24, r = t - ocq * 24;
     const bool active = (t < 384);
-
     for (int i = t; i < 784; i += NT) xs[i] = x[n * 784 + i];
     for (int i = t; i < 288; i += NT) w1s[i] = w1[i];
-
     float acc[4][24];
 #pragma unroll
     for (int j = 0; j < 4; ++j)
 #pragma unroll
         for (int xo = 0; xo < 24; ++xo) acc[j][xo] = 0.f;
-
     for (int ic = 0; ic < 32; ++ic) {
         __syncthreads();
         float bb1 = b1[ic];
@@ -501,7 +822,6 @@
     }
     __syncthreads();
 }
-
 __global__ __launch_bounds__(512) void fused_kernel(
     const float* __restrict__ x, const float* __restrict__ w1, const float* __restrict__ b1,
     const float* __restrict__ w2, const float* __restrict__ b2,
@@ -522,9 +842,7 @@
     __shared__ float red[8][10];
     __shared__ float evs[10];
     const int n = blockIdx.x, t = threadIdx.x;
-
     conv_stage<512>(buf, n, t, x, w1, b1, w2, b2);
-
     {
         const int j = t >> 2, q = t & 3;
         const float* wrow = fw1 + (size_t)j * 9216 + q * 2304;
@@ -602,8 +920,8 @@
         convnet_mfma<<<1024, 256, 0, stream>>>(x, w1, b1, w2t, b2, flat);
         fc1_mfma<<<dim3(16, 2, 16), 256, 0, stream>>>(flat, fw1h, part);
         fc2_kernel<<<1024, 128, 0, stream>>>(part, fb1, fw2, fb2, angb);
-        circuit_kernel<<<1024, 512, 0, stream>>>(angb, qrx, qrz3, qps6, qrot7, qmrz8,
-                                                 qcrx9, qcry10, qcrz11, qu2, qu3, out);
+        circuit_wave<<<256, 256, 0, stream>>>(angb, qrx, qrz3, qps6, qrot7, qmrz8,
+                                              qcrx9, qcry10, qcrz11, qu2, qu3, out);
     } else {
         fused_kernel<<<1024, 512, 0, stream>>>(x, w1, b1, w2, b2, fw1, fb1, fw2, fb2,
                                                qrx, qrz3, qps6, qrot7, qmrz8,
```

New measurement: 283.4 us. +38.4%, slower.
